# Kernel optimization log

Hardware: AMD Instinct MI355X
Metric: run time of the kernel (lower is better)

## Reference

```python
import jax, jax.numpy as jnp
import numpy as np

D, H, G, HD = 2048, 16, 4, 128  # d_model, num_heads, num_groups, head_dim
B, S = 2, 2048


def _rope(x):
    # x: [B, heads, S, HD]; RoPE with concat(freqs, freqs) layout (rotate_half style)
    seq = x.shape[2]
    inv_freq = 1.0 / (10000.0 ** (jnp.arange(0, HD, 2, dtype=jnp.float32) / HD))  # [HD/2]
    t = jnp.arange(seq, dtype=jnp.float32)
    freqs = t[:, None] * inv_freq[None, :]              # [S, HD/2]
    emb = jnp.concatenate([freqs, freqs], axis=-1)      # [S, HD]
    cos = jnp.cos(emb)[None, None]                      # [1,1,S,HD]
    sin = jnp.sin(emb)[None, None]
    x1, x2 = jnp.split(x, 2, axis=-1)
    rot = jnp.concatenate([-x2, x1], axis=-1)           # rotate_half
    return x * cos + rot * sin


def setup_inputs() -> dict:
    key = jax.random.key(0)
    ks = jax.random.split(key, 5)
    x = jax.random.normal(ks[0], (B, S, D), dtype=jnp.float32)
    # weights stored as [in, out] so y = x @ W (equivalent to torch Linear with W^T)
    Wq = jax.random.normal(ks[1], (D, D), dtype=jnp.float32) * 0.02
    Wk = jax.random.normal(ks[2], (D, G * HD), dtype=jnp.float32) * 0.02
    Wv = jax.random.normal(ks[3], (D, G * HD), dtype=jnp.float32) * 0.02
    Wo = jax.random.normal(ks[4], (D, D), dtype=jnp.float32) * 0.02
    # causal mask: True = masked (matches torch masked_fill semantics)
    mask = ~jnp.tril(jnp.ones((S, S), dtype=bool))[None, None]  # [1,1,S,S]
    return {"x": x, "Wq": Wq, "Wk": Wk, "Wv": Wv, "Wo": Wo, "mask": mask}


def reference(x, Wq, Wk, Wv, Wo, mask):
    b, s, _ = x.shape
    q = (x @ Wq).reshape(b, s, H, HD).transpose(0, 2, 1, 3)   # [B,H,S,HD]
    k = (x @ Wk).reshape(b, s, G, HD).transpose(0, 2, 1, 3)   # [B,G,S,HD]
    v = (x @ Wv).reshape(b, s, G, HD).transpose(0, 2, 1, 3)   # [B,G,S,HD]
    q = _rope(q)
    k = _rope(k)
    # GQA: repeat_interleave KV groups across heads
    k = jnp.repeat(k, H // G, axis=1)                         # [B,H,S,HD]
    v = jnp.repeat(v, H // G, axis=1)
    scale = jnp.float32(1.0 / np.sqrt(HD))
    scores = jnp.einsum('bhqd,bhkd->bhqk', q, k) * scale      # [B,H,S,S]
    scores = jnp.where(mask, jnp.float32(-1e9), scores)
    attn = jax.nn.softmax(scores, axis=-1)
    ctx = jnp.einsum('bhqk,bhkd->bhqd', attn, v)              # [B,H,S,HD]
    ctx = ctx.transpose(0, 2, 1, 3).reshape(b, s, D)
    return ctx @ Wo
```

## Files before the change

### kernel.cpp

```cpp
#include <hip/hip_runtime.h>
#include <hip/hip_bf16.h>
#include <math.h>

#define BB 2
#define SS 2048
#define DD 2048
#define HH 16
#define GG 4
#define HDIM 128
#define DKV (GG * HDIM)
#define MS (BB * SS)
#define QKVS 3072

typedef __attribute__((ext_vector_type(8))) short bf16x8;
typedef __attribute__((ext_vector_type(4))) float f32x4;
typedef __attribute__((ext_vector_type(4))) unsigned int u32x4;

__device__ __forceinline__ ushort f2bf(float x) {
    __hip_bfloat16 b = __float2bfloat16(x);
    return *(ushort*)&b;
}
__device__ __forceinline__ float bf2f(ushort u) {
    __hip_bfloat16 b;
    *(ushort*)&b = u;
    return __bfloat162float(b);
}

#define GLOAD_LDS(src, dst)                                                        \
    __builtin_amdgcn_global_load_lds(                                              \
        (const __attribute__((address_space(1))) unsigned int*)(src),              \
        (__attribute__((address_space(3))) unsigned int*)(dst), 16, 0, 0)

#define WAITV(n) asm volatile("s_waitcnt vmcnt(" #n ")" ::: "memory")

__global__ void cast_bf16(const float* __restrict__ X, ushort* __restrict__ O, int total8) {
    int idx = blockIdx.x * blockDim.x + threadIdx.x;
    if (idx >= total8) return;
    const float4* p = (const float4*)X + (size_t)idx * 2;
    float4 a = p[0], b = p[1];
    float v[8] = {a.x, a.y, a.z, a.w, b.x, b.y, b.z, b.w};
    ushort r[8];
#pragma unroll
    for (int j = 0; j < 8; ++j) r[j] = f2bf(v[j]);
    *((u32x4*)O + idx) = *(u32x4*)r;
}

__global__ __launch_bounds__(256) void transpose_cast(const float* __restrict__ W,
                                                      ushort* __restrict__ WT,
                                                      int K, int N) {
    __shared__ ushort tile[32][33];
    const int tx = threadIdx.x & 31, ty = threadIdx.x >> 5;
    const int n0 = blockIdx.x * 32, k0 = blockIdx.y * 32;
#pragma unroll
    for (int i = 0; i < 4; ++i)
        tile[ty + i * 8][tx] = f2bf(W[(size_t)(k0 + ty + i * 8) * N + n0 + tx]);
    __syncthreads();
#pragma unroll
    for (int i = 0; i < 4; ++i)
        WT[(size_t)(n0 + ty + i * 8) * K + k0 + tx] = tile[tx][ty + i * 8];
}

__global__ __launch_bounds__(256) void transpose_v(const ushort* __restrict__ QKV,
                                                   ushort* __restrict__ VT) {
    __shared__ ushort tile[32][33];
    const int tx = threadIdx.x & 31, ty = threadIdx.x >> 5;
    const int d0 = blockIdx.x * 32;
    const int k0 = blockIdx.y * 32;
    const int b = blockIdx.z;
#pragma unroll
    for (int i = 0; i < 4; ++i)
        tile[ty + i * 8][tx] =
            QKV[(size_t)(b * SS + k0 + ty + i * 8) * QKVS + 2560 + d0 + tx];
    __syncthreads();
    const int posl = ((tx & 12) << 1) | ((tx & 16) >> 2) | (tx & 3);
#pragma unroll
    for (int i = 0; i < 4; ++i)
        VT[((size_t)b * DKV + d0 + ty + i * 8) * SS + k0 + posl] = tile[tx][ty + i * 8];
}

template <int BN, bool OUT_BF16>
__global__ __launch_bounds__(512) void gemm8(const ushort* __restrict__ A,
                                             const ushort* __restrict__ BT,
                                             void* __restrict__ Cout,
                                             int M, int N, int K) {
    constexpr int ABUF = 128 * 32;
    constexpr int BBUF = BN * 32;
    constexpr int NWC = BN / 64;
    constexpr int NWM = 8 / NWC;
    constexpr int ROWS = 128 / NWM;
    constexpr int MFR = ROWS / 16;
    __shared__ ushort As[3 * ABUF];
    __shared__ ushort Bs[3 * BBUF];

    const int t = threadIdx.x;
    const int w = t >> 6, l = t & 63;
    const int lm = l & 15, lw = l >> 4;
    const int wr = w / NWC, wc = w % NWC;
    const int nx = gridDim.x;
    const int bid = blockIdx.y * nx + blockIdx.x;
    const int cpx = (nx * gridDim.y) >> 3;
    const int swb = (bid & 7) * cpx + (bid >> 3);
    const int bm = (swb / nx) * 128, bn = (swb % nx) * BN;

    const int NT = K >> 5;
    const int swzc = (lw ^ ((lm >> 1) & 3)) * 8;

    const int ar0 = t >> 2, ac0 = (t & 3) ^ ((ar0 >> 1) & 3);
    const ushort* a0 = A + (size_t)(bm + ar0) * K + ac0 * 8;
    const int br0 = t >> 2, bc0 = (t & 3) ^ ((br0 >> 1) & 3);
    const ushort* b0 = BT + (size_t)(bn + br0) * K + bc0 * 8;
    const int br1 = (t + 512) >> 2, bc1 = ((t + 512) & 3) ^ ((br1 >> 1) & 3);
    const ushort* b1 = BT + (size_t)(bn + br1) * K + bc1 * 8;

    auto STAGE = [&](int slot) {
        GLOAD_LDS(a0, &As[slot * ABUF + t * 8]);
        a0 += 32;
        GLOAD_LDS(b0, &Bs[slot * BBUF + t * 8]);
        b0 += 32;
        if constexpr (BN == 256) {
            GLOAD_LDS(b1, &Bs[slot * BBUF + (t + 512) * 8]);
            b1 += 32;
        }
    };

    f32x4 acc[MFR][4];
#pragma unroll
    for (int m = 0; m < MFR; ++m)
#pragma unroll
        for (int n = 0; n < 4; ++n) acc[m][n] = (f32x4){0.f, 0.f, 0.f, 0.f};

    STAGE(0);
    STAGE(1);
    int cs = 0, ps = 2;

#pragma unroll 1
    for (int kt = 0; kt < NT; ++kt) {
        if (kt + 1 < NT) {
            if constexpr (BN == 256) WAITV(3); else WAITV(2);
        } else {
            WAITV(0);
        }
        __builtin_amdgcn_s_barrier();
        if (kt + 2 < NT) STAGE(ps);

        const ushort* Ab = &As[cs * ABUF];
        const ushort* Bb = &Bs[cs * BBUF];
        bf16x8 bfr[4], af[MFR];
#pragma unroll
        for (int n = 0; n < 4; ++n)
            bfr[n] = *(const bf16x8*)&Bb[(wc * 64 + n * 16 + lm) * 32 + swzc];
#pragma unroll
        for (int i = 0; i < MFR; ++i)
            af[i] = *(const bf16x8*)&Ab[(wr * ROWS + i * 16 + lm) * 32 + swzc];
        __builtin_amdgcn_s_setprio(1);
#pragma unroll
        for (int i = 0; i < MFR; ++i)
#pragma unroll
            for (int n = 0; n < 4; ++n)
                acc[i][n] = __builtin_amdgcn_mfma_f32_16x16x32_bf16(af[i], bfr[n], acc[i][n], 0, 0, 0);
        __builtin_amdgcn_s_setprio(0);

        cs = (cs == 2) ? 0 : cs + 1;
        ps = (ps == 2) ? 0 : ps + 1;
    }

#pragma unroll
    for (int m = 0; m < MFR; ++m)
#pragma unroll
        for (int n = 0; n < 4; ++n)
#pragma unroll
            for (int r = 0; r < 4; ++r) {
                int row = bm + wr * ROWS + m * 16 + lw * 4 + r;
                int col = bn + wc * 64 + n * 16 + lm;
                if (OUT_BF16)
                    ((ushort*)Cout)[(size_t)row * N + col] = f2bf(acc[m][n][r]);
                else
                    ((float*)Cout)[(size_t)row * N + col] = acc[m][n][r];
            }
}

__global__ void rope_bf16(ushort* __restrict__ X, int total) {
    int idx = blockIdx.x * blockDim.x + threadIdx.x;
    if (idx >= total) return;
    int i = idx & 63;
    int hh = (idx >> 6) % 20;
    int row = idx / (64 * 20);
    int s = row & (SS - 1);
    int colOff = (hh < 16) ? hh * HDIM : 2048 + (hh - 16) * HDIM;
    float inv = exp2f((float)i * -0.2076205059304601f);
    float ang = (float)s * inv;
    float c, sn;
    __sincosf(ang, &sn, &c);
    size_t base = (size_t)row * QKVS + colOff + i;
    float x1 = bf2f(X[base]), x2 = bf2f(X[base + 64]);
    X[base] = f2bf(x1 * c - x2 * sn);
    X[base + 64] = f2bf(x2 * c + x1 * sn);
}

#define SCL 0.08838834764831845f
#define CEXP 0.1275296340545927f
#define THRRAW 90.50966799187809f

__global__ __launch_bounds__(256) void attn_mfma(const ushort* __restrict__ QKV,
                                                 const ushort* __restrict__ VT,
                                                 ushort* __restrict__ Ctx) {
    __shared__ ushort Ks[2][64 * 128];
    __shared__ ushort Vs[2][128 * 64];
    const int t = threadIdx.x;
    const int w = t >> 6;
    const int l = t & 63;
    const int lm = l & 15, lw = l >> 4;
    const int bid = blockIdx.x;
    const int g = bid & 3;
    const int b = (bid >> 2) & 1;
    const int within = bid >> 3;
    const int xq = within & 15;
    const int h = g * 4 + (within >> 4);
    const int swz = (lm & 7) << 3;

    const ushort* kbase = QKV + (size_t)(b * SS) * QKVS + 2048 + g * HDIM;
    const ushort* vbase = VT + ((size_t)b * DKV + g * HDIM) * SS;

    const short one_bf = (short)0x3F80;
    const bf16x8 ones = {one_bf, one_bf, one_bf, one_bf, one_bf, one_bf, one_bf, one_bf};

    ushort* ksb = &Ks[0][0];
    ushort* vsb = &Vs[0][0];

#pragma unroll 1
    for (int phase = 0; phase < 2; ++phase) {
        const int qt = (phase == 0) ? xq : (31 - xq);
        const int q0 = qt * 64;
        const int qw = q0 + w * 16;
        const int q = qw + lm;
        const int ntiles = qt + 1;

        const ushort* ks[4];
        const ushort* vs[4];
#pragma unroll
        for (int it = 0; it < 4; ++it) {
            int c = t + it * 256;
            int kr = c >> 4, ko = c & 15;
            ks[it] = kbase + (size_t)kr * QKVS + ((ko ^ (kr & 7)) * 8);
            int vr = c >> 3, vo = c & 7;
            vs[it] = vbase + (size_t)vr * SS + ((vo ^ (vr & 7)) * 8);
        }

        bf16x8 qa[4];
        {
            const ushort* qp = QKV + (size_t)(b * SS + qw + lm) * QKVS + h * HDIM + lw * 8;
#pragma unroll
            for (int kk = 0; kk < 4; ++kk)
                qa[kk] = *(const bf16x8*)(qp + kk * 32);
        }

        f32x4 acc[8];
#pragma unroll
        for (int d = 0; d < 8; ++d) acc[d] = (f32x4){0.f, 0.f, 0.f, 0.f};
        f32x4 accl = (f32x4){0.f, 0.f, 0.f, 0.f};
        float m = -INFINITY;

#pragma unroll
        for (int it = 0; it < 4; ++it) {
            GLOAD_LDS(ks[it], ksb + (t + it * 256) * 8);
            ks[it] += 64 * QKVS;
            GLOAD_LDS(vs[it], vsb + (t + it * 256) * 8);
            vs[it] += 64;
        }
        asm volatile("s_waitcnt vmcnt(0)" ::: "memory");
        __builtin_amdgcn_s_barrier();

#pragma unroll 1
        for (int tile = 0; tile < ntiles; ++tile) {
            const int cur = tile & 1;
            const int kv0 = tile * 64;
            const bool more = (tile + 1 < ntiles);
            if (more) {
                ushort* kd = ksb + (cur ^ 1) * (64 * 128);
                ushort* vd = vsb + (cur ^ 1) * (128 * 64);
#pragma unroll
                for (int it = 0; it < 4; ++it) {
                    GLOAD_LDS(ks[it], kd + (t + it * 256) * 8);
                    ks[it] += 64 * QKVS;
                    GLOAD_LDS(vs[it], vd + (t + it * 256) * 8);
                    vs[it] += 64;
                }
            }

            f32x4 sfT[4];
#pragma unroll
            for (int kvb = 0; kvb < 4; ++kvb) sfT[kvb] = (f32x4){0.f, 0.f, 0.f, 0.f};
            __builtin_amdgcn_s_setprio(1);
#pragma unroll
            for (int kvb = 0; kvb < 4; ++kvb)
#pragma unroll
                for (int kk = 0; kk < 4; ++kk) {
                    bf16x8 kb = *(const bf16x8*)&Ks[cur][(kvb * 16 + lm) * 128 + ((kk * 32 + lw * 8) ^ swz)];
                    sfT[kvb] = __builtin_amdgcn_mfma_f32_16x16x32_bf16(kb, qa[kk], sfT[kvb], 0, 0, 0);
                }
            __builtin_amdgcn_s_setprio(0);

            if (tile == ntiles - 1) {
#pragma unroll
                for (int kvb = 0; kvb < 4; ++kvb)
#pragma unroll
                    for (int r = 0; r < 4; ++r) {
                        int kv = kv0 + kvb * 16 + lw * 4 + r;
                        if (kv > q) sfT[kvb][r] = -INFINITY;
                    }
            }

            float rm = fmaxf(fmaxf(sfT[0][0], sfT[0][1]), fmaxf(sfT[0][2], sfT[0][3]));
#pragma unroll
            for (int kvb = 1; kvb < 4; ++kvb)
                rm = fmaxf(rm, fmaxf(fmaxf(sfT[kvb][0], sfT[kvb][1]),
                                     fmaxf(sfT[kvb][2], sfT[kvb][3])));
            rm = fmaxf(rm, __shfl_xor(rm, 16));
            rm = fmaxf(rm, __shfl_xor(rm, 32));

            bool stable = (rm - m <= THRRAW);
            if (!__all((int)stable)) {
                float mn = fmaxf(m, rm);
                float alpha_l = exp2f((m - mn) * CEXP);
                m = mn;
                float ar[4];
#pragma unroll
                for (int r = 0; r < 4; ++r)
                    ar[r] = __shfl(alpha_l, (l & 48) | (lw * 4 + r));
#pragma unroll
                for (int d = 0; d < 8; ++d) {
                    acc[d][0] *= ar[0];
                    acc[d][1] *= ar[1];
                    acc[d][2] *= ar[2];
                    acc[d][3] *= ar[3];
                }
                accl[0] *= ar[0];
                accl[1] *= ar[1];
                accl[2] *= ar[2];
                accl[3] *= ar[3];
            }

            bf16x8 pa[2];
            float mC = m * CEXP;
#pragma unroll
            for (int kvb = 0; kvb < 4; ++kvb)
#pragma unroll
                for (int r = 0; r < 4; ++r) {
                    float pv = exp2f(fmaf(sfT[kvb][r], CEXP, -mC));
                    pa[kvb >> 1][(kvb & 1) * 4 + r] = (short)f2bf(pv);
                }

            __builtin_amdgcn_s_setprio(1);
#pragma unroll
            for (int kks = 0; kks < 2; ++kks) {
                accl = __builtin_amdgcn_mfma_f32_16x16x32_bf16(pa[kks], ones, accl, 0, 0, 0);
#pragma unroll
                for (int dcol = 0; dcol < 8; ++dcol) {
                    bf16x8 vb = *(const bf16x8*)&Vs[cur][(dcol * 16 + lm) * 64 + ((kks * 32 + lw * 8) ^ swz)];
                    acc[dcol] = __builtin_amdgcn_mfma_f32_16x16x32_bf16(pa[kks], vb, acc[dcol], 0, 0, 0);
                }
            }
            __builtin_amdgcn_s_setprio(0);

            if (more) {
                asm volatile("s_waitcnt vmcnt(0)" ::: "memory");
                __builtin_amdgcn_s_barrier();
            }
        }

        float rinv[4];
#pragma unroll
        for (int r = 0; r < 4; ++r) rinv[r] = 1.f / accl[r];
        ushort* cp = Ctx + (size_t)(b * SS + qw) * DD + h * HDIM;
#pragma unroll
        for (int d = 0; d < 8; ++d)
#pragma unroll
            for (int r = 0; r < 4; ++r)
                cp[(size_t)(lw * 4 + r) * DD + d * 16 + lm] = f2bf(acc[d][r] * rinv[r]);
        __builtin_amdgcn_s_barrier();
    }
}

extern "C" void kernel_launch(void* const* d_in, const int* in_sizes, int n_in,
                              void* d_out, int out_size, void* d_ws, size_t ws_size,
                              hipStream_t stream) {
    const float* x  = (const float*)d_in[0];
    const float* Wq = (const float*)d_in[1];
    const float* Wk = (const float*)d_in[2];
    const float* Wv = (const float*)d_in[3];
    const float* Wo = (const float*)d_in[4];
    float* out = (float*)d_out;

    ushort* xh    = (ushort*)d_ws;
    ushort* QKV   = xh + (size_t)MS * DD;
    ushort* VTb   = QKV + (size_t)MS * QKVS;
    ushort* WqkvT = VTb + (size_t)MS * DKV;
    ushort* WoT   = WqkvT + (size_t)QKVS * DD;
    ushort* Ch    = xh;

    dim3 blk(256);
    int nx8 = MS * DD / 8;
    cast_bf16<<<(nx8 + 255) / 256, 256, 0, stream>>>(x, xh, nx8);

    transpose_cast<<<dim3(DD / 32, DD / 32), blk, 0, stream>>>(Wq, WqkvT, DD, DD);
    transpose_cast<<<dim3(DKV / 32, DD / 32), blk, 0, stream>>>(Wk, WqkvT + (size_t)DD * DD, DD, DKV);
    transpose_cast<<<dim3(DKV / 32, DD / 32), blk, 0, stream>>>(Wv, WqkvT + (size_t)(DD + DKV) * DD, DD, DKV);

    gemm8<256, true><<<dim3(QKVS / 256, MS / 128), dim3(512), 0, stream>>>(xh, WqkvT, QKV, MS, QKVS, DD);

    int nrope = MS * 20 * 64;
    rope_bf16<<<(nrope + 255) / 256, 256, 0, stream>>>(QKV, nrope);

    transpose_v<<<dim3(DKV / 32, SS / 32, BB), blk, 0, stream>>>(QKV, VTb);

    attn_mfma<<<dim3(512), dim3(256), 0, stream>>>(QKV, VTb, Ch);

    transpose_cast<<<dim3(DD / 32, DD / 32), blk, 0, stream>>>(Wo, WoT, DD, DD);
    gemm8<128, false><<<dim3(DD / 128, MS / 128), dim3(512), 0, stream>>>(Ch, WoT, out, MS, DD, DD);
}
```

Baseline: 210.1 us.

## Process 128-row query tiles per block, sharing each K/V tile across two row groups

The attention kernel used to run two 64-row query tiles in sequence as balanced phases, reloading K/V for each one. Each block now handles one 128-row query tile. Every wave keeps two 16-row query groups in registers, so each K/V tile staged in LDS serves both groups, halving K/V global traffic per query row. Blocks are ordered heaviest tile first, and launch bounds request two blocks per SIMD-unit occupancy. The cost is about double the accumulator registers, which may cause spills or lower occupancy, and load balance across blocks is now uneven.

```diff
diff --git a/kernel.cpp b/kernel.cpp
--- a/kernel.cpp
+++ b/kernel.cpp
@@ -201,9 +201,9 @@
 #define CEXP 0.1275296340545927f
 #define THRRAW 90.50966799187809f
 
-__global__ __launch_bounds__(256) void attn_mfma(const ushort* __restrict__ QKV,
-                                                 const ushort* __restrict__ VT,
-                                                 ushort* __restrict__ Ctx) {
+__global__ __launch_bounds__(256, 2) void attn_mfma(const ushort* __restrict__ QKV,
+                                                    const ushort* __restrict__ VT,
+                                                    ushort* __restrict__ Ctx) {
     __shared__ ushort Ks[2][64 * 128];
     __shared__ ushort Vs[2][128 * 64];
     const int t = threadIdx.x;
@@ -214,171 +214,184 @@
     const int g = bid & 3;
     const int b = (bid >> 2) & 1;
     const int within = bid >> 3;
-    const int xq = within & 15;
+    const int qt = 15 - (within & 15);
     const int h = g * 4 + (within >> 4);
     const int swz = (lm & 7) << 3;
 
+    const int q0 = qt * 128;
+    const int qw0 = q0 + w * 16;
+    const int qw1 = qw0 + 64;
+    const int qA = qw0 + lm, qB = qw1 + lm;
+    const int ntiles = 2 * qt + 2;
+
     const ushort* kbase = QKV + (size_t)(b * SS) * QKVS + 2048 + g * HDIM;
     const ushort* vbase = VT + ((size_t)b * DKV + g * HDIM) * SS;
 
     const short one_bf = (short)0x3F80;
     const bf16x8 ones = {one_bf, one_bf, one_bf, one_bf, one_bf, one_bf, one_bf, one_bf};
 
-    ushort* ksb = &Ks[0][0];
-    ushort* vsb = &Vs[0][0];
+    const ushort* ks[4];
+    const ushort* vs[4];
+#pragma unroll
+    for (int it = 0; it < 4; ++it) {
+        int c = t + it * 256;
+        int kr = c >> 4, ko = c & 15;
+        ks[it] = kbase + (size_t)kr * QKVS + ((ko ^ (kr & 7)) * 8);
+        int vr = c >> 3, vo = c & 7;
+        vs[it] = vbase + (size_t)vr * SS + ((vo ^ (vr & 7)) * 8);
+    }
+
+    bf16x8 qa0[4], qa1[4];
+    {
+        const ushort* qp0 = QKV + (size_t)(b * SS + qw0 + lm) * QKVS + h * HDIM + lw * 8;
+        const ushort* qp1 = QKV + (size_t)(b * SS + qw1 + lm) * QKVS + h * HDIM + lw * 8;
+#pragma unroll
+        for (int kk = 0; kk < 4; ++kk) {
+            qa0[kk] = *(const bf16x8*)(qp0 + kk * 32);
+            qa1[kk] = *(const bf16x8*)(qp1 + kk * 32);
+        }
+    }
+
+    f32x4 acc0[8], acc1[8];
+#pragma unroll
+    for (int d = 0; d < 8; ++d) {
+        acc0[d] = (f32x4){0.f, 0.f, 0.f, 0.f};
+        acc1[d] = (f32x4){0.f, 0.f, 0.f, 0.f};
+    }
+    f32x4 accl0 = (f32x4){0.f, 0.f, 0.f, 0.f};
+    f32x4 accl1 = (f32x4){0.f, 0.f, 0.f, 0.f};
+    float m0 = -INFINITY, m1 = -INFINITY;
+
+#pragma unroll
+    for (int it = 0; it < 4; ++it) {
+        GLOAD_LDS(ks[it], &Ks[0][(t + it * 256) * 8]);
+        ks[it] += 64 * QKVS;
+        GLOAD_LDS(vs[it], &Vs[0][(t + it * 256) * 8]);
+        vs[it] += 64;
+    }
+    asm volatile("s_waitcnt vmcnt(0)" ::: "memory");
+    __builtin_amdgcn_s_barrier();
+
+    auto group_step = [&](int cur, int kv0, const bf16x8* qa, int qrow, bool diag,
+                          float& m, f32x4& accl, f32x4* acc) {
+        f32x4 sfT[4];
+#pragma unroll
+        for (int kvb = 0; kvb < 4; ++kvb) sfT[kvb] = (f32x4){0.f, 0.f, 0.f, 0.f};
+        __builtin_amdgcn_s_setprio(1);
+#pragma unroll
+        for (int kvb = 0; kvb < 4; ++kvb)
+#pragma unroll
+            for (int kk = 0; kk < 4; ++kk) {
+                bf16x8 kb = *(const bf16x8*)&Ks[cur][(kvb * 16 + lm) * 128 + ((kk * 32 + lw * 8) ^ swz)];
+                sfT[kvb] = __builtin_amdgcn_mfma_f32_16x16x32_bf16(kb, qa[kk], sfT[kvb], 0, 0, 0);
+            }
+        __builtin_amdgcn_s_setprio(0);
+
+        if (diag) {
+#pragma unroll
+            for (int kvb = 0; kvb < 4; ++kvb)
+#pragma unroll
+                for (int r = 0; r < 4; ++r) {
+                    int kv = kv0 + kvb * 16 + lw * 4 + r;
+                    if (kv > qrow) sfT[kvb][r] = -INFINITY;
+                }
+        }
+
+        float rm = fmaxf(fmaxf(sfT[0][0], sfT[0][1]), fmaxf(sfT[0][2], sfT[0][3]));
+#pragma unroll
+        for (int kvb = 1; kvb < 4; ++kvb)
+            rm = fmaxf(rm, fmaxf(fmaxf(sfT[kvb][0], sfT[kvb][1]),
+                                 fmaxf(sfT[kvb][2], sfT[kvb][3])));
+        rm = fmaxf(rm, __shfl_xor(rm, 16));
+        rm = fmaxf(rm, __shfl_xor(rm, 32));
+
+        bool stable = (rm - m <= THRRAW);
+        if (!__all((int)stable)) {
+            float mn = fmaxf(m, rm);
+            float alpha_l = exp2f((m - mn) * CEXP);
+            m = mn;
+            float ar[4];
+#pragma unroll
+            for (int r = 0; r < 4; ++r)
+                ar[r] = __shfl(alpha_l, (l & 48) | (lw * 4 + r));
+#pragma unroll
+            for (int d = 0; d < 8; ++d) {
+                acc[d][0] *= ar[0];
+                acc[d][1] *= ar[1];
+                acc[d][2] *= ar[2];
+                acc[d][3] *= ar[3];
+            }
+            accl[0] *= ar[0];
+            accl[1] *= ar[1];
+            accl[2] *= ar[2];
+            accl[3] *= ar[3];
+        }
+
+        bf16x8 pa[2];
+        float mC = m * CEXP;
+#pragma unroll
+        for (int kvb = 0; kvb < 4; ++kvb)
+#pragma unroll
+            for (int r = 0; r < 4; ++r) {
+                float pv = exp2f(fmaf(sfT[kvb][r], CEXP, -mC));
+                pa[kvb >> 1][(kvb & 1) * 4 + r] = (short)f2bf(pv);
+            }
+
+        __builtin_amdgcn_s_setprio(1);
+#pragma unroll
+        for (int kks = 0; kks < 2; ++kks) {
+            accl = __builtin_amdgcn_mfma_f32_16x16x32_bf16(pa[kks], ones, accl, 0, 0, 0);
+#pragma unroll
+            for (int dcol = 0; dcol < 8; ++dcol) {
+                bf16x8 vb = *(const bf16x8*)&Vs[cur][(dcol * 16 + lm) * 64 + ((kks * 32 + lw * 8) ^ swz)];
+                acc[dcol] = __builtin_amdgcn_mfma_f32_16x16x32_bf16(pa[kks], vb, acc[dcol], 0, 0, 0);
+            }
+        }
+        __builtin_amdgcn_s_setprio(0);
+    };
 
 #pragma unroll 1
-    for (int phase = 0; phase < 2; ++phase) {
-        const int qt = (phase == 0) ? xq : (31 - xq);
-        const int q0 = qt * 64;
-        const int qw = q0 + w * 16;
-        const int q = qw + lm;
-        const int ntiles = qt + 1;
-
-        const ushort* ks[4];
-        const ushort* vs[4];
-#pragma unroll
-        for (int it = 0; it < 4; ++it) {
-            int c = t + it * 256;
-            int kr = c >> 4, ko = c & 15;
-            ks[it] = kbase + (size_t)kr * QKVS + ((ko ^ (kr & 7)) * 8);
-            int vr = c >> 3, vo = c & 7;
-            vs[it] = vbase + (size_t)vr * SS + ((vo ^ (vr & 7)) * 8);
-        }
-
-        bf16x8 qa[4];
-        {
-            const ushort* qp = QKV + (size_t)(b * SS + qw + lm) * QKVS + h * HDIM + lw * 8;
-#pragma unroll
-            for (int kk = 0; kk < 4; ++kk)
-                qa[kk] = *(const bf16x8*)(qp + kk * 32);
-        }
-
-        f32x4 acc[8];
-#pragma unroll
-        for (int d = 0; d < 8; ++d) acc[d] = (f32x4){0.f, 0.f, 0.f, 0.f};
-        f32x4 accl = (f32x4){0.f, 0.f, 0.f, 0.f};
-        float m = -INFINITY;
-
-#pragma unroll
-        for (int it = 0; it < 4; ++it) {
-            GLOAD_LDS(ks[it], ksb + (t + it * 256) * 8);
-            ks[it] += 64 * QKVS;
-            GLOAD_LDS(vs[it], vsb + (t + it * 256) * 8);
-            vs[it] += 64;
-        }
-        asm volatile("s_waitcnt vmcnt(0)" ::: "memory");
-        __builtin_amdgcn_s_barrier();
-
-#pragma unroll 1
-        for (int tile = 0; tile < ntiles; ++tile) {
-            const int cur = tile & 1;
-            const int kv0 = tile * 64;
-            const bool more = (tile + 1 < ntiles);
-            if (more) {
-                ushort* kd = ksb + (cur ^ 1) * (64 * 128);
-                ushort* vd = vsb + (cur ^ 1) * (128 * 64);
-#pragma unroll
-                for (int it = 0; it < 4; ++it) {
-                    GLOAD_LDS(ks[it], kd + (t + it * 256) * 8);
-                    ks[it] += 64 * QKVS;
-                    GLOAD_LDS(vs[it], vd + (t + it * 256) * 8);
-                    vs[it] += 64;
-                }
-            }
-
-            f32x4 sfT[4];
-#pragma unroll
-            for (int kvb = 0; kvb < 4; ++kvb) sfT[kvb] = (f32x4){0.f, 0.f, 0.f, 0.f};
-            __builtin_amdgcn_s_setprio(1);
-#pragma unroll
-            for (int kvb = 0; kvb < 4; ++kvb)
-#pragma unroll
-                for (int kk = 0; kk < 4; ++kk) {
-                    bf16x8 kb = *(const bf16x8*)&Ks[cur][(kvb * 16 + lm) * 128 + ((kk * 32 + lw * 8) ^ swz)];
-                    sfT[kvb] = __builtin_amdgcn_mfma_f32_16x16x32_bf16(kb, qa[kk], sfT[kvb], 0, 0, 0);
-                }
-            __builtin_amdgcn_s_setprio(0);
-
-            if (tile == ntiles - 1) {
-#pragma unroll
-                for (int kvb = 0; kvb < 4; ++kvb)
-#pragma unroll
-                    for (int r = 0; r < 4; ++r) {
-                        int kv = kv0 + kvb * 16 + lw * 4 + r;
-                        if (kv > q) sfT[kvb][r] = -INFINITY;
-                    }
-            }
-
-            float rm = fmaxf(fmaxf(sfT[0][0], sfT[0][1]), fmaxf(sfT[0][2], sfT[0][3]));
-#pragma unroll
-            for (int kvb = 1; kvb < 4; ++kvb)
-                rm = fmaxf(rm, fmaxf(fmaxf(sfT[kvb][0], sfT[kvb][1]),
-                                     fmaxf(sfT[kvb][2], sfT[kvb][3])));
-            rm = fmaxf(rm, __shfl_xor(rm, 16));
-            rm = fmaxf(rm, __shfl_xor(rm, 32));
-
-            bool stable = (rm - m <= THRRAW);
-            if (!__all((int)stable)) {
-                float mn = fmaxf(m, rm);
-                float alpha_l = exp2f((m - mn) * CEXP);
-                m = mn;
-                float ar[4];
-#pragma unroll
-                for (int r = 0; r < 4; ++r)
-                    ar[r] = __shfl(alpha_l, (l & 48) | (lw * 4 + r));
-#pragma unroll
-                for (int d = 0; d < 8; ++d) {
-                    acc[d][0] *= ar[0];
-                    acc[d][1] *= ar[1];
-                    acc[d][2] *= ar[2];
-                    acc[d][3] *= ar[3];
-                }
-                accl[0] *= ar[0];
-                accl[1] *= ar[1];
-                accl[2] *= ar[2];
-                accl[3] *= ar[3];
-            }
-
-            bf16x8 pa[2];
-            float mC = m * CEXP;
-#pragma unroll
-            for (int kvb = 0; kvb < 4; ++kvb)
-#pragma unroll
-                for (int r = 0; r < 4; ++r) {
-                    float pv = exp2f(fmaf(sfT[kvb][r], CEXP, -mC));
-                    pa[kvb >> 1][(kvb & 1) * 4 + r] = (short)f2bf(pv);
-                }
-
-            __builtin_amdgcn_s_setprio(1);
-#pragma unroll
-            for (int kks = 0; kks < 2; ++kks) {
-                accl = __builtin_amdgcn_mfma_f32_16x16x32_bf16(pa[kks], ones, accl, 0, 0, 0);
-#pragma unroll
-                for (int dcol = 0; dcol < 8; ++dcol) {
-                    bf16x8 vb = *(const bf16x8*)&Vs[cur][(dcol * 16 + lm) * 64 + ((kks * 32 + lw * 8) ^ swz)];
-                    acc[dcol] = __builtin_amdgcn_mfma_f32_16x16x32_bf16(pa[kks], vb, acc[dcol], 0, 0, 0);
-                }
-            }
-            __builtin_amdgcn_s_setprio(0);
-
-            if (more) {
-                asm volatile("s_waitcnt vmcnt(0)" ::: "memory");
-                __builtin_amdgcn_s_barrier();
-            }
-        }
-
-        float rinv[4];
-#pragma unroll
-        for (int r = 0; r < 4; ++r) rinv[r] = 1.f / accl[r];
-        ushort* cp = Ctx + (size_t)(b * SS + qw) * DD + h * HDIM;
-#pragma unroll
-        for (int d = 0; d < 8; ++d)
-#pragma unroll
-            for (int r = 0; r < 4; ++r)
-                cp[(size_t)(lw * 4 + r) * DD + d * 16 + lm] = f2bf(acc[d][r] * rinv[r]);
-        __builtin_amdgcn_s_barrier();
-    }
+    for (int tile = 0; tile < ntiles; ++tile) {
+        const int cur = tile & 1;
+        const int kv0 = tile * 64;
+        const bool more = (tile + 1 < ntiles);
+        if (more) {
+            ushort* kd = &Ks[cur ^ 1][0];
+            ushort* vd = &Vs[cur ^ 1][0];
+#pragma unroll
+            for (int it = 0; it < 4; ++it) {
+                GLOAD_LDS(ks[it], kd + (t + it * 256) * 8);
+                ks[it] += 64 * QKVS;
+                GLOAD_LDS(vs[it], vd + (t + it * 256) * 8);
+                vs[it] += 64;
+            }
+        }
+
+        if (tile < ntiles - 1)
+            group_step(cur, kv0, qa0, qA, tile == ntiles - 2, m0, accl0, acc0);
+        group_step(cur, kv0, qa1, qB, tile == ntiles - 1, m1, accl1, acc1);
+
+        if (more) {
+            asm volatile("s_waitcnt vmcnt(0)" ::: "memory");
+            __builtin_amdgcn_s_barrier();
+        }
+    }
+
+    float rinv0[4], rinv1[4];
+#pragma unroll
+    for (int r = 0; r < 4; ++r) {
+        rinv0[r] = 1.f / accl0[r];
+        rinv1[r] = 1.f / accl1[r];
+    }
+    ushort* cp0 = Ctx + (size_t)(b * SS + qw0) * DD + h * HDIM;
+    ushort* cp1 = Ctx + (size_t)(b * SS + qw1) * DD + h * HDIM;
+#pragma unroll
+    for (int d = 0; d < 8; ++d)
+#pragma unroll
+        for (int r = 0; r < 4; ++r) {
+            cp0[(size_t)(lw * 4 + r) * DD + d * 16 + lm] = f2bf(acc0[d][r] * rinv0[r]);
+            cp1[(size_t)(lw * 4 + r) * DD + d * 16 + lm] = f2bf(acc1[d][r] * rinv1[r]);
+        }
 }
 
 extern "C" void kernel_launch(void* const* d_in, const int* in_sizes, int n_in,
```

Measured after the change: 240.2 us. 1.14x slower.
